# Kernel optimization log

Measured on AMD Instinct MI355X. Metric: run time of the kernel, lower is better.

The kernel has to match this reference:

```python
import jax, jax.numpy as jnp
import numpy as np

B, T, FD, NH, NC, NOUT = 32, 512, 256, 1024, 512, 8


def setup_inputs() -> dict:
    key = jax.random.key(0)
    ks = jax.random.split(key, 12)
    s = lambda k, sh, sc=0.05: (jax.random.normal(k, sh, jnp.float32) * sc)
    return dict(
        x=jax.random.normal(ks[0], (B, T, FD), jnp.float32),
        lens=jax.random.randint(ks[1], (B,), T // 2, T + 1, jnp.int32),
        W1=s(ks[2], (NH, FD)), b1=jnp.zeros((NH,), jnp.float32),
        g1=jnp.ones((NH,), jnp.float32), be1=jnp.zeros((NH,), jnp.float32),
        W2=s(ks[3], (NH, NH)), b2=jnp.zeros((NH,), jnp.float32),
        g2=jnp.ones((NH,), jnp.float32), be2=jnp.zeros((NH,), jnp.float32),
        lstm_wih=s(ks[4], (2, 2, 4 * NC, NH)),   # [layer, dir, 4H, in]
        lstm_whh=s(ks[5], (2, 2, 4 * NC, NC)),   # [layer, dir, 4H, H]
        lstm_bih=s(ks[6], (2, 2, 4 * NC)),
        lstm_bhh=s(ks[7], (2, 2, 4 * NC)),
        w_u=s(ks[8], (2 * NC,)), b_u=jnp.zeros((), jnp.float32),
        Wc=s(ks[9], (NOUT, 2 * NC)), bc=jnp.zeros((NOUT,), jnp.float32),
    )


def _layernorm(x, g, b, eps=1e-5):
    m = x.mean(-1, keepdims=True)
    v = ((x - m) ** 2).mean(-1, keepdims=True)
    return (x - m) / jnp.sqrt(v + eps) * g + b


def _lrelu(z):
    return jnp.where(z >= 0, z, 0.01 * z)  # LeakyReLU default slope


def _lstm_dir(x, wih, whh, bih, bhh):
    # x: [B,T,in] -> h: [B,T,H]; torch gate order i,f,g,o
    Bz = x.shape[0]
    H = whh.shape[1]
    xp = jnp.einsum('bti,gi->btg', x, wih) + bih + bhh  # [B,T,4H]

    def step(carry, xt):
        h, c = carry
        gates = xt + h @ whh.T
        i, f, g, o = jnp.split(gates, 4, axis=-1)
        c = jax.nn.sigmoid(f) * c + jax.nn.sigmoid(i) * jnp.tanh(g)
        h = jax.nn.sigmoid(o) * jnp.tanh(c)
        return (h, c), h

    h0 = jnp.zeros((Bz, H), x.dtype)
    _, hs = jax.lax.scan(step, (h0, h0), xp.transpose(1, 0, 2))
    return hs.transpose(1, 0, 2)


def _bilstm(x, wih, whh, bih, bhh):
    # params indexed [dir, ...]; backward dir processes the full padded
    # sequence reversed (original feeds unpacked pad_sequence to nn.LSTM)
    hf = _lstm_dir(x, wih[0], whh[0], bih[0], bhh[0])
    hb = _lstm_dir(x[:, ::-1], wih[1], whh[1], bih[1], bhh[1])[:, ::-1]
    return jnp.concatenate([hf, hb], axis=-1)


def reference(x, lens, W1, b1, g1, be1, W2, b2, g2, be2,
              lstm_wih, lstm_whh, lstm_bih, lstm_bhh, w_u, b_u, Wc, bc):
    Tn = x.shape[1]
    # extract MLP (dropout = identity in eval)
    h = _lrelu(_layernorm(x @ W1.T + b1, g1, be1))
    h = _lrelu(_layernorm(h @ W2.T + b2, g2, be2))
    # pad_sequence zero-pads AFTER extract -> zero out pad positions
    mask = jnp.arange(Tn)[None, :] < lens[:, None]  # [B,T]
    h = h * mask[..., None]
    # 2-layer bidirectional LSTM over the full padded sequence
    h = _bilstm(h, lstm_wih[0], lstm_whh[0], lstm_bih[0], lstm_bhh[0])
    h = _bilstm(h, lstm_wih[1], lstm_whh[1], lstm_bih[1], lstm_bhh[1])
    # Attn with window_len=1: per-step linear score, masked softmax, weighted sum
    scores = h @ w_u + b_u                          # [B,T]
    scores = jnp.where(mask, scores, -jnp.inf)
    alpha = jax.nn.softmax(scores, axis=-1)
    pooled = jnp.einsum('bt,btd->bd', alpha, h)     # [B, 2*NC]
    return pooled @ Wc.T + bc
```

## Files before the change

kernel.cpp:

```cpp
#include <hip/hip_runtime.h>
#include <stdint.h>
#include <stddef.h>


typedef short  short8  __attribute__((ext_vector_type(8)));
typedef short  short4v __attribute__((ext_vector_type(4)));
typedef float  float4v __attribute__((ext_vector_type(4)));
typedef unsigned long long u64;

__device__ inline float b2f(short x){
  union { unsigned u; float f; } v; v.u = ((unsigned)(unsigned short)x) << 16; return v.f;
}
__device__ inline short f2b(float f){
  union { float f; unsigned u; } v; v.f = f;
  unsigned r = (v.u + 0x7fffu + ((v.u >> 16) & 1u)) >> 16;
  return (short)r;
}
__device__ inline float sigm(float x){ return 1.f / (1.f + __expf(-x)); }
__device__ inline float tanh_(float x){ return 2.f / (1.f + __expf(-2.f*x)) - 1.f; }

__global__ __launch_bounds__(256) void detect_f32(
    const unsigned short* __restrict__ p, unsigned* __restrict__ flag)
{
  const int tid = threadIdx.x;
  unsigned h = 0;
  for (int i = tid; i < 1024; i += 256){
    const unsigned e = (p[i] >> 7) & 0xFFu;
    if (e >= 0xC0u) ++h;
  }
#pragma unroll
  for (int off=32; off>0; off>>=1) h += __shfl_xor(h, off, 64);
  __shared__ unsigned sh[4];
  if ((tid&63)==0) sh[tid>>6] = h;
  __syncthreads();
  if (tid==0) *flag = (sh[0]+sh[1]+sh[2]+sh[3] >= 8u) ? 1u : 0u;
}

__global__ __launch_bounds__(256) void to_bf16(
    const void* __restrict__ src, short* __restrict__ dst, int n,
    const unsigned* __restrict__ flag)
{
  const int i = blockIdx.x*256 + threadIdx.x;
  if (i >= n) return;
  if (*flag) dst[i] = f2b(((const float*)src)[i]);
  else       dst[i] = ((const short*)src)[i];
}

__global__ __launch_bounds__(256) void to_bf16_perm(
    const void* __restrict__ src, short* __restrict__ dst, const int W,
    const int n, const unsigned* __restrict__ flag)
{
  const int i = blockIdx.x*256 + threadIdx.x;
  if (i >= n) return;
  const int col = i % W;
  const int r   = (i / W) % 2048;
  const int blk = i / (W * 2048);
  const int gate = r >> 9, unit = r & 511;
  const size_t j = ((size_t)blk*2048 + (size_t)(unit*4 + gate))*W + col;
  short out = (*flag) ? f2b(((const float*)src)[i]) : ((const short*)src)[i];
  dst[j] = out;
}

__global__ __launch_bounds__(256) void gemm_bt(
    const short* __restrict__ A, const short* __restrict__ W,
    short* __restrict__ C, const short* __restrict__ bias1,
    const short* __restrict__ bias2, int N, int K)
{
  __shared__ __align__(16) short lA[128*40];
  __shared__ __align__(16) short lW[128*40];
  const int tid  = threadIdx.x;
  const int lane = tid & 63, wv = tid >> 6;
  const int wm = wv >> 1, wn = wv & 1;
  const int quad = lane >> 4, l15 = lane & 15;
  const long m0 = (long)blockIdx.y * 128, n0 = (long)blockIdx.x * 128;

  float4v acc[4][4];
#pragma unroll
  for (int i=0;i<4;++i)
#pragma unroll
    for (int j=0;j<4;++j) acc[i][j] = (float4v)0.f;

  const int r  = tid >> 2;
  const int kc = tid & 3;
  const int nkt = K >> 5;
  for (int kt = 0; kt < nkt; ++kt) {
    __syncthreads();
    const short* ga = A + (m0 + r) * (long)K + kt*32 + kc*8;
    const short* gw = W + (n0 + r) * (long)K + kt*32 + kc*8;
    short8 a0 = *(const short8*)ga;
    short8 a1 = *(const short8*)(ga + 64*(long)K);
    short8 w0 = *(const short8*)gw;
    short8 w1 = *(const short8*)(gw + 64*(long)K);
    *(short8*)&lA[r*40 + kc*8]        = a0;
    *(short8*)&lA[(r+64)*40 + kc*8]   = a1;
    *(short8*)&lW[r*40 + kc*8]        = w0;
    *(short8*)&lW[(r+64)*40 + kc*8]   = w1;
    __syncthreads();
    short8 af[4], bfr[4];
#pragma unroll
    for (int i=0;i<4;++i) af[i]  = *(const short8*)&lA[(wm*64 + i*16 + l15)*40 + quad*8];
#pragma unroll
    for (int j=0;j<4;++j) bfr[j] = *(const short8*)&lW[(wn*64 + j*16 + l15)*40 + quad*8];
#pragma unroll
    for (int i=0;i<4;++i)
#pragma unroll
      for (int j=0;j<4;++j)
        acc[i][j] = __builtin_amdgcn_mfma_f32_16x16x32_bf16(af[i], bfr[j], acc[i][j], 0, 0, 0);
  }
#pragma unroll
  for (int j=0;j<4;++j){
    const long n = n0 + wn*64 + j*16 + l15;
    float bs = b2f(bias1[n]);
    if (bias2) bs += b2f(bias2[n]);
#pragma unroll
    for (int i=0;i<4;++i){
      const long mb = m0 + wm*64 + i*16 + quad*4;
#pragma unroll
      for (int g=0; g<4; ++g)
        C[(mb+g)*(long)N + n] = f2b(acc[i][j][g] + bs);
    }
  }
}

__global__ __launch_bounds__(256) void ln_lrelu(
    const short* __restrict__ X, const short* __restrict__ g,
    const short* __restrict__ be, short* __restrict__ out,
    const int* __restrict__ lens, const int domask)
{
  const int row = blockIdx.x, tid = threadIdx.x;
  const short* xr = X + (size_t)row * 1024;
  short4v xv = *(const short4v*)(xr + tid*4);
  float v[4];
#pragma unroll
  for (int k=0;k<4;++k) v[k] = b2f(xv[k]);
  float s  = v[0]+v[1]+v[2]+v[3];
  float sq = v[0]*v[0]+v[1]*v[1]+v[2]*v[2]+v[3]*v[3];
#pragma unroll
  for (int off=32; off>0; off>>=1){
    s  += __shfl_xor(s,  off, 64);
    sq += __shfl_xor(sq, off, 64);
  }
  __shared__ float red[8];
  if ((tid&63)==0){ red[tid>>6] = s; red[4+(tid>>6)] = sq; }
  __syncthreads();
  s  = red[0]+red[1]+red[2]+red[3];
  sq = red[4]+red[5]+red[6]+red[7];
  const float mean = s * (1.f/1024.f);
  const float var  = sq * (1.f/1024.f) - mean*mean;
  const float rstd = rsqrtf(var + 1e-5f);
  float zmul = 1.f;
  if (domask){ const int b = row >> 9, t = row & 511; if (t >= lens[b]) zmul = 0.f; }
  short4v o;
#pragma unroll
  for (int k=0;k<4;++k){
    const int n = tid*4 + k;
    float y = (v[k]-mean)*rstd*b2f(g[n]) + b2f(be[n]);
    y = (y >= 0.f) ? y : 0.01f*y;
    o[k] = f2b(y * zmul);
  }
  *(short4v*)(out + (size_t)row*1024 + tid*4) = o;
}

__global__ __launch_bounds__(256) void lstm_scan(
    const short* __restrict__ xp, const int xp_cols, const int dir0,
    const short* __restrict__ whh,
    u64* __restrict__ hstate,
    short* __restrict__ hout,
    const unsigned epoch)
{
  const int wg = blockIdx.x;
  const int dloc = wg >> 5, d = dir0 + dloc;
  const int u0 = (wg & 31) * 16;
  const int tid = threadIdx.x, lane = tid & 63, wv = tid >> 6;
  const int quad = lane >> 4, l15 = lane & 15;

  short8 af[16];
  {
    const int prow = (u0 + wv*4)*4 + l15;
    const short* wr = whh + ((size_t)d*2048 + prow)*512 + quad*8;
#pragma unroll
    for (int ks=0; ks<16; ++ks) af[ks] = *(const short8*)(wr + ks*32);
  }

  float cstA = 0.f, cstB = 0.f;
  __shared__ __align__(16) unsigned hsh[2][32*260];
  const unsigned tbase = epoch << 10;
  const int pair = (u0 >> 1) + wv*2 + (quad >> 1);

  const size_t gb = (size_t)dloc*2048 + (size_t)(u0 + wv*4 + quad)*4;
  const short* xpA = xp + (size_t)l15*512*xp_cols + gb;
  const short* xpB = xp + (size_t)(l15+16)*512*xp_cols + gb;

  short4v xc0, xc1;
  {
    const int t0 = d ? 511 : 0;
    xc0 = *(const short4v*)(xpA + (size_t)t0*xp_cols);
    xc1 = *(const short4v*)(xpB + (size_t)t0*xp_cols);
  }

  for (int step=0; step<512; ++step){
    const int t = d ? (511-step) : step;
    short4v xn0 = (short4v)0, xn1 = (short4v)0;
    unsigned* stg = &hsh[step&1][tid];
    if (step == 0){
      const int tn = d ? 510 : 1;
      xn0 = *(const short4v*)(xpA + (size_t)tn*xp_cols);
      xn1 = *(const short4v*)(xpB + (size_t)tn*xp_cols);
#pragma unroll
      for (int k=0;k<32;++k) stg[k*260] = 0u;
    } else {
      const u64* hq = hstate + ((size_t)(d*2 + (step&1))<<13) + tid;
      const unsigned tgt = tbase + (unsigned)step;
      u64 v[32];
      for(;;){
        unsigned ok = 1u;
#pragma unroll
        for (int k=0;k<32;++k)
          v[k] = __hip_atomic_load(hq + (size_t)k*256,
                                   __ATOMIC_RELAXED, __HIP_MEMORY_SCOPE_AGENT);
#pragma unroll
        for (int k=0;k<32;++k) ok &= (unsigned)((unsigned)(v[k] >> 32) == tgt);
        if (ok) break;
        for(;;){
          u64 s0 = __hip_atomic_load(hq, __ATOMIC_RELAXED,
                                     __HIP_MEMORY_SCOPE_AGENT);
          if ((unsigned)(s0 >> 32) == tgt) break;
          __builtin_amdgcn_s_sleep(1);
        }
      }
      if (step < 511){
        const int tn = d ? (510-step) : (step+1);
        xn0 = *(const short4v*)(xpA + (size_t)tn*xp_cols);
        xn1 = *(const short4v*)(xpB + (size_t)tn*xp_cols);
      }
#pragma unroll
      for (int k=0;k<32;++k) stg[k*260] = (unsigned)v[k];
    }
    __syncthreads();

    float4v a0e, a0o, a1e, a1o;
#pragma unroll
    for (int g=0; g<4; ++g){
      a0e[g] = b2f(xc0[g]); a1e[g] = b2f(xc1[g]);
      a0o[g] = 0.f;         a1o[g] = 0.f;
    }
    const short* hs = (const short*)&hsh[step&1][0];
#pragma unroll
    for (int kp=0; kp<8; ++kp){
      short8 b0e = *(const short8*)(hs + (size_t)l15*520      + (2*kp)*32   + quad*8);
      short8 b0o = *(const short8*)(hs + (size_t)l15*520      + (2*kp+1)*32 + quad*8);
      short8 b1e = *(const short8*)(hs + (size_t)(l15+16)*520 + (2*kp)*32   + quad*8);
      short8 b1o = *(const short8*)(hs + (size_t)(l15+16)*520 + (2*kp+1)*32 + quad*8);
      a0e = __builtin_amdgcn_mfma_f32_16x16x32_bf16(af[2*kp],   b0e, a0e, 0, 0, 0);
      a0o = __builtin_amdgcn_mfma_f32_16x16x32_bf16(af[2*kp+1], b0o, a0o, 0, 0, 0);
      a1e = __builtin_amdgcn_mfma_f32_16x16x32_bf16(af[2*kp],   b1e, a1e, 0, 0, 0);
      a1o = __builtin_amdgcn_mfma_f32_16x16x32_bf16(af[2*kp+1], b1o, a1o, 0, 0, 0);
    }

    u64* hdst = hstate + ((size_t)(d*2 + ((step+1)&1))<<13);
    const u64 tag = (u64)(tbase + (unsigned)step + 1u) << 32;

    {
      const float gi = a0e[0]+a0o[0], gf = a0e[1]+a0o[1];
      const float gg = a0e[2]+a0o[2], go = a0e[3]+a0o[3];
      cstA = sigm(gf)*cstA + sigm(gi)*tanh_(gg);
      const float h0 = sigm(go)*tanh_(cstA);
      const unsigned h0u = (unsigned)(unsigned short)f2b(h0);
      const unsigned o0  = __shfl_xor(h0u, 16, 64);
      if ((quad & 1) == 0){
        const unsigned pay = h0u | (o0 << 16);
        __hip_atomic_store(hdst + (size_t)l15*256 + pair, tag | pay,
                           __ATOMIC_RELAXED, __HIP_MEMORY_SCOPE_AGENT);
        *(unsigned*)&hout[((size_t)l15*512 + t)*1024 + d*512 + 2*pair] = pay;
      }
    }
    {
      const float gi = a1e[0]+a1o[0], gf = a1e[1]+a1o[1];
      const float gg = a1e[2]+a1o[2], go = a1e[3]+a1o[3];
      cstB = sigm(gf)*cstB + sigm(gi)*tanh_(gg);
      const float h1 = sigm(go)*tanh_(cstB);
      const unsigned h1u = (unsigned)(unsigned short)f2b(h1);
      const unsigned o1  = __shfl_xor(h1u, 16, 64);
      if (quad & 1){
        const unsigned pay = (o1 & 0xFFFFu) | (h1u << 16);
        __hip_atomic_store(hdst + (size_t)(l15+16)*256 + pair, tag | pay,
                           __ATOMIC_RELAXED, __HIP_MEMORY_SCOPE_AGENT);
        *(unsigned*)&hout[((size_t)(l15+16)*512 + t)*1024 + d*512 + 2*pair] = pay;
      }
    }
    xc0 = xn0; xc1 = xn1;
  }
}

__global__ __launch_bounds__(256) void attn_cls(
    const short* __restrict__ hseq, const short* __restrict__ wu,
    const short* __restrict__ Wc, const short* __restrict__ bc,
    const int* __restrict__ lens, float* __restrict__ out)
{
  const int b = blockIdx.x, tid = threadIdx.x, lane = tid & 63, wv = tid >> 6;
  const int len = lens[b];
  __shared__ float wus[1024];
  __shared__ float sc[512];
  __shared__ float redx[8];
  __shared__ float pooled[1024];
  for (int i=tid; i<1024; i+=256) wus[i] = b2f(wu[i]);
  __syncthreads();
  const short* hb = hseq + (size_t)b*512*1024;
  for (int t=wv; t<512; t+=4){
    const short* hr = hb + (size_t)t*1024;
    float s = 0.f;
#pragma unroll
    for (int j=0;j<16;++j) s += b2f(hr[lane + j*64]) * wus[lane + j*64];
#pragma unroll
    for (int off=32; off>0; off>>=1) s += __shfl_xor(s, off, 64);
    if (lane==0) sc[t] = (t < len) ? s : -3.0e38f;
  }
  __syncthreads();
  float m = -3.0e38f;
  for (int i=tid;i<512;i+=256) m = fmaxf(m, sc[i]);
#pragma unroll
  for (int off=32; off>0; off>>=1) m = fmaxf(m, __shfl_xor(m, off, 64));
  if (lane==0) redx[wv] = m;
  __syncthreads();
  m = fmaxf(fmaxf(redx[0],redx[1]), fmaxf(redx[2],redx[3]));
  float ssum = 0.f;
  for (int i=tid;i<512;i+=256){
    float e = (i<len) ? __expf(sc[i]-m) : 0.f;
    sc[i] = e;
    ssum += e;
  }
#pragma unroll
  for (int off=32; off>0; off>>=1) ssum += __shfl_xor(ssum, off, 64);
  if (lane==0) redx[4+wv] = ssum;
  __syncthreads();
  ssum = redx[4]+redx[5]+redx[6]+redx[7];
  const float inv = 1.f/ssum;
  float4v pa = (float4v)0.f;
  const int k0 = tid*4;
  for (int t=0; t<len; ++t){
    const float a = sc[t];
    short4v hv = *(const short4v*)(hb + (size_t)t*1024 + k0);
    pa[0] += a*b2f(hv[0]); pa[1] += a*b2f(hv[1]);
    pa[2] += a*b2f(hv[2]); pa[3] += a*b2f(hv[3]);
  }
  pooled[k0+0] = pa[0]*inv; pooled[k0+1] = pa[1]*inv;
  pooled[k0+2] = pa[2]*inv; pooled[k0+3] = pa[3]*inv;
  __syncthreads();
  const int j = tid >> 5, l32 = tid & 31;
  float s2 = 0.f;
  for (int kk=l32; kk<1024; kk+=32) s2 += b2f(Wc[j*1024+kk]) * pooled[kk];
#pragma unroll
  for (int off=16; off>0; off>>=1) s2 += __shfl_xor(s2, off, 32);
  if (l32==0) out[b*8+j] = s2 + b2f(bc[j]);
}

extern "C" void kernel_launch(void* const* d_in, const int* in_sizes, int n_in,
                              void* d_out, int out_size, void* d_ws, size_t ws_size,
                              hipStream_t stream)
{
  (void)in_sizes; (void)n_in; (void)out_size;
  const int*   lens = (const int*)d_in[1];
  float* outp = (float*)d_out;

  const size_t SZ_XP_A = (size_t)16384*4096*2;
  const size_t SZ_XP_B = (size_t)16384*2048*2;
  const size_t SZ_H    = (size_t)16384*1024*2;
  const size_t SZ_HS   = 262144;
  const size_t SZ_CNT  = 16384;
  const size_t SZ_NORM = 37000000;
  const bool planA = ws_size >= SZ_XP_A + 2*SZ_H + SZ_HS + SZ_CNT + SZ_NORM;
  const bool planB = !planA && ws_size >= SZ_XP_B + 2*SZ_H + SZ_HS + SZ_CNT + SZ_NORM;
  if (!planA && !planB) return;
  const size_t xpsz = planA ? SZ_XP_A : SZ_XP_B;

  char* ws = (char*)d_ws;
  short*    XP  = (short*)ws;
  short*    HB  = (short*)(ws + xpsz);
  short*    HC  = (short*)(ws + xpsz + SZ_H);
  u64*      HS64= (u64*)(ws + xpsz + 2*SZ_H);
  unsigned* CNT = (unsigned*)(ws + xpsz + 2*SZ_H + SZ_HS);
  unsigned* FLAG = CNT + 4000;
  short*    pool = (short*)(ws + xpsz + 2*SZ_H + SZ_HS + SZ_CNT);

  size_t off = 0;
  auto carve = [&](size_t n){ short* p = pool + off; off += (n + 127) & ~(size_t)127; return p; };
  short* x   = carve(4194304);
  short* W1  = carve(262144);
  short* b1  = carve(1024);
  short* g1  = carve(1024);
  short* be1 = carve(1024);
  short* W2  = carve(1048576);
  short* b2  = carve(1024);
  short* g2  = carve(1024);
  short* be2 = carve(1024);
  short* wih = carve(8388608);
  short* whh = carve(4194304);
  short* bih = carve(8192);
  short* bhh = carve(8192);
  short* wu  = carve(1024);
  short* Wc  = carve(8192);
  short* bc  = carve(8);

  hipMemsetAsync(HS64, 0, SZ_HS, stream);
  detect_f32<<<1, 256, 0, stream>>>((const unsigned short*)d_in[0], FLAG);

  struct { int idx; short* dst; int n; } cv[12] = {
    {0,x,4194304},{2,W1,262144},{3,b1,1024},{4,g1,1024},{5,be1,1024},
    {6,W2,1048576},{7,b2,1024},{8,g2,1024},{9,be2,1024},
    {14,wu,1024},{16,Wc,8192},{17,bc,8}
  };
  for (int i=0;i<12;++i)
    to_bf16<<<(cv[i].n + 255)/256, 256, 0, stream>>>(d_in[cv[i].idx], cv[i].dst, cv[i].n, FLAG);
  struct { int idx; short* dst; int W; int n; } pv[4] = {
    {10,wih,1024,8388608},{11,whh,512,4194304},{12,bih,1,8192},{13,bhh,1,8192}
  };
  for (int i=0;i<4;++i)
    to_bf16_perm<<<(pv[i].n + 255)/256, 256, 0, stream>>>(d_in[pv[i].idx], pv[i].dst,
                                                          pv[i].W, pv[i].n, FLAG);

  dim3 blk(256);
  gemm_bt<<<dim3(8,128),  blk, 0, stream>>>(x,  W1, XP, b1, nullptr, 1024, 256);
  ln_lrelu<<<16384, blk, 0, stream>>>(XP, g1, be1, HB, lens, 0);
  gemm_bt<<<dim3(8,128),  blk, 0, stream>>>(HB, W2, XP, b2, nullptr, 1024, 1024);
  ln_lrelu<<<16384, blk, 0, stream>>>(XP, g2, be2, HC, lens, 1);

  const short* lin[2]  = { HC, HB };
  short*       lout[2] = { HB, HC };
  for (int l = 0; l < 2; ++l){
    const short* whh_l = whh + (size_t)l*2*2048*512;
    if (planA){
      gemm_bt<<<dim3(32,128), blk, 0, stream>>>(
          lin[l], wih + (size_t)l*4096*1024, XP,
          bih + l*4096, bhh + l*4096, 4096, 1024);
      lstm_scan<<<64, blk, 0, stream>>>(XP, 4096, 0, whh_l, HS64, lout[l],
                                        (unsigned)(l+1));
    } else {
      for (int d = 0; d < 2; ++d){
        gemm_bt<<<dim3(16,128), blk, 0, stream>>>(
            lin[l], wih + ((size_t)(l*2+d))*2048*1024, XP,
            bih + (l*2+d)*2048, bhh + (l*2+d)*2048, 2048, 1024);
        lstm_scan<<<32, blk, 0, stream>>>(XP, 2048, d, whh_l, HS64, lout[l],
                                          (unsigned)(l+1));
      }
    }
  }
  attn_cls<<<32, blk, 0, stream>>>(HC, wu, Wc, bc, lens, outp);
}
```

Measured before the change: 4.552 ms.

## Split recurrent step into two batch halves to overlap polling with MFMA

The per-step wait on the shared hidden state is split into two halves of 16 batch rows. The first half is polled and staged before computing its gates, while loads for the second half are issued and then finished after the first half's MFMA and cell update. This hides part of the cross-block synchronisation latency behind compute, pipelining the two batch halves. The cost is an extra __syncthreads per step and a busier polling loop without sleep for the second half.

```diff
diff --git a/kernel.cpp b/kernel.cpp
--- a/kernel.cpp
+++ b/kernel.cpp
@@ -200,66 +200,53 @@
 
   for (int step=0; step<512; ++step){
     const int t = d ? (511-step) : step;
-    short4v xn0 = (short4v)0, xn1 = (short4v)0;
     unsigned* stg = &hsh[step&1][tid];
+    const u64* hq = hstate + ((size_t)(d*2 + (step&1))<<13) + tid;
+    const unsigned tgt = tbase + (unsigned)step;
+
     if (step == 0){
-      const int tn = d ? 510 : 1;
-      xn0 = *(const short4v*)(xpA + (size_t)tn*xp_cols);
-      xn1 = *(const short4v*)(xpB + (size_t)tn*xp_cols);
-#pragma unroll
-      for (int k=0;k<32;++k) stg[k*260] = 0u;
+#pragma unroll
+      for (int k=0;k<16;++k) stg[k*260] = 0u;
     } else {
-      const u64* hq = hstate + ((size_t)(d*2 + (step&1))<<13) + tid;
-      const unsigned tgt = tbase + (unsigned)step;
-      u64 v[32];
+      u64 v[16];
       for(;;){
         unsigned ok = 1u;
 #pragma unroll
-        for (int k=0;k<32;++k)
+        for (int k=0;k<16;++k)
           v[k] = __hip_atomic_load(hq + (size_t)k*256,
                                    __ATOMIC_RELAXED, __HIP_MEMORY_SCOPE_AGENT);
 #pragma unroll
-        for (int k=0;k<32;++k) ok &= (unsigned)((unsigned)(v[k] >> 32) == tgt);
+        for (int k=0;k<16;++k) ok &= (unsigned)((unsigned)(v[k] >> 32) == tgt);
         if (ok) break;
-        for(;;){
-          u64 s0 = __hip_atomic_load(hq, __ATOMIC_RELAXED,
-                                     __HIP_MEMORY_SCOPE_AGENT);
-          if ((unsigned)(s0 >> 32) == tgt) break;
-          __builtin_amdgcn_s_sleep(1);
-        }
+        __builtin_amdgcn_s_sleep(1);
       }
-      if (step < 511){
-        const int tn = d ? (510-step) : (step+1);
-        xn0 = *(const short4v*)(xpA + (size_t)tn*xp_cols);
-        xn1 = *(const short4v*)(xpB + (size_t)tn*xp_cols);
-      }
-#pragma unroll
-      for (int k=0;k<32;++k) stg[k*260] = (unsigned)v[k];
+#pragma unroll
+      for (int k=0;k<16;++k) stg[k*260] = (unsigned)v[k];
     }
     __syncthreads();
 
-    float4v a0e, a0o, a1e, a1o;
-#pragma unroll
-    for (int g=0; g<4; ++g){
-      a0e[g] = b2f(xc0[g]); a1e[g] = b2f(xc1[g]);
-      a0o[g] = 0.f;         a1o[g] = 0.f;
-    }
+    u64 vb[16];
+    if (step > 0){
+#pragma unroll
+      for (int k=0;k<16;++k)
+        vb[k] = __hip_atomic_load(hq + (size_t)(16+k)*256,
+                                  __ATOMIC_RELAXED, __HIP_MEMORY_SCOPE_AGENT);
+    }
+
+    float4v a0e, a0o;
+#pragma unroll
+    for (int g=0; g<4; ++g){ a0e[g] = b2f(xc0[g]); a0o[g] = 0.f; }
     const short* hs = (const short*)&hsh[step&1][0];
 #pragma unroll
     for (int kp=0; kp<8; ++kp){
-      short8 b0e = *(const short8*)(hs + (size_t)l15*520      + (2*kp)*32   + quad*8);
-      short8 b0o = *(const short8*)(hs + (size_t)l15*520      + (2*kp+1)*32 + quad*8);
-      short8 b1e = *(const short8*)(hs + (size_t)(l15+16)*520 + (2*kp)*32   + quad*8);
-      short8 b1o = *(const short8*)(hs + (size_t)(l15+16)*520 + (2*kp+1)*32 + quad*8);
+      short8 b0e = *(const short8*)(hs + (size_t)l15*520 + (2*kp)*32   + quad*8);
+      short8 b0o = *(const short8*)(hs + (size_t)l15*520 + (2*kp+1)*32 + quad*8);
       a0e = __builtin_amdgcn_mfma_f32_16x16x32_bf16(af[2*kp],   b0e, a0e, 0, 0, 0);
       a0o = __builtin_amdgcn_mfma_f32_16x16x32_bf16(af[2*kp+1], b0o, a0o, 0, 0, 0);
-      a1e = __builtin_amdgcn_mfma_f32_16x16x32_bf16(af[2*kp],   b1e, a1e, 0, 0, 0);
-      a1o = __builtin_amdgcn_mfma_f32_16x16x32_bf16(af[2*kp+1], b1o, a1o, 0, 0, 0);
     }
 
     u64* hdst = hstate + ((size_t)(d*2 + ((step+1)&1))<<13);
     const u64 tag = (u64)(tbase + (unsigned)step + 1u) << 32;
-
     {
       const float gi = a0e[0]+a0o[0], gf = a0e[1]+a0o[1];
       const float gg = a0e[2]+a0o[2], go = a0e[3]+a0o[3];
@@ -273,6 +260,42 @@
                            __ATOMIC_RELAXED, __HIP_MEMORY_SCOPE_AGENT);
         *(unsigned*)&hout[((size_t)l15*512 + t)*1024 + d*512 + 2*pair] = pay;
       }
+    }
+
+    if (step == 0){
+#pragma unroll
+      for (int k=0;k<16;++k) stg[(16+k)*260] = 0u;
+    } else {
+      for(;;){
+        unsigned ok = 1u;
+#pragma unroll
+        for (int k=0;k<16;++k) ok &= (unsigned)((unsigned)(vb[k] >> 32) == tgt);
+        if (ok) break;
+#pragma unroll
+        for (int k=0;k<16;++k)
+          vb[k] = __hip_atomic_load(hq + (size_t)(16+k)*256,
+                                    __ATOMIC_RELAXED, __HIP_MEMORY_SCOPE_AGENT);
+      }
+#pragma unroll
+      for (int k=0;k<16;++k) stg[(16+k)*260] = (unsigned)vb[k];
+    }
+    short4v xn0 = (short4v)0, xn1 = (short4v)0;
+    if (step < 511){
+      const int tn = d ? (510-step) : (step+1);
+      xn0 = *(const short4v*)(xpA + (size_t)tn*xp_cols);
+      xn1 = *(const short4v*)(xpB + (size_t)tn*xp_cols);
+    }
+    __syncthreads();
+
+    float4v a1e, a1o;
+#pragma unroll
+    for (int g=0; g<4; ++g){ a1e[g] = b2f(xc1[g]); a1o[g] = 0.f; }
+#pragma unroll
+    for (int kp=0; kp<8; ++kp){
+      short8 b1e = *(const short8*)(hs + (size_t)(l15+16)*520 + (2*kp)*32   + quad*8);
+      short8 b1o = *(const short8*)(hs + (size_t)(l15+16)*520 + (2*kp+1)*32 + quad*8);
+      a1e = __builtin_amdgcn_mfma_f32_16x16x32_bf16(af[2*kp],   b1e, a1e, 0, 0, 0);
+      a1o = __builtin_amdgcn_mfma_f32_16x16x32_bf16(af[2*kp+1], b1o, a1o, 0, 0, 0);
     }
     {
       const float gi = a1e[0]+a1o[0], gf = a1e[1]+a1o[1];
```

After: 4.862 ms. 1.07x slower.
